# Kernel tuning notes

Measured on AMD Instinct MI355X. Metric: run time of the kernel, lower is better.

Reference implementation:

```python
import jax, jax.numpy as jnp
import numpy as np

N, E, C, Z, NB, NG, NL = 4000, 48000, 64, 10, 8, 8, 2
R_MAX = 5.0
P = 5.0  # polynomial cutoff power
AVG_NEIGH = 12.0
# l-index of each of the 16 spherical-harmonic components (l = 0..3)
ELLS = np.concatenate([[0], [1] * 3, [2] * 5, [3] * 7])


def _sph(u):
    # component-normalized real spherical harmonics up to l=3, u: unit vectors [E,3]
    x, y, z = u[..., 0], u[..., 1], u[..., 2]
    s3 = np.sqrt(3.0); s5 = np.sqrt(5.0); s15 = np.sqrt(15.0)
    s7 = np.sqrt(7.0); s105 = np.sqrt(105.0)
    s35_8 = np.sqrt(35.0 / 8.0); s21_8 = np.sqrt(21.0 / 8.0)
    x2, y2, z2 = x * x, y * y, z * z
    return jnp.stack([
        jnp.ones_like(x),
        s3 * x, s3 * y, s3 * z,
        s15 * x * y, s15 * y * z, 0.5 * s5 * (3.0 * z2 - 1.0), s15 * x * z, 0.5 * s15 * (x2 - y2),
        s35_8 * y * (3.0 * x2 - y2), s105 * x * y * z, s21_8 * y * (5.0 * z2 - 1.0),
        0.5 * s7 * z * (5.0 * z2 - 3.0), s21_8 * x * (5.0 * z2 - 1.0),
        0.5 * s105 * z * (x2 - y2), s35_8 * x * (x2 - 3.0 * y2),
    ], axis=-1)


def _radial(r):
    # Bessel radial basis * polynomial cutoff envelope; r: [E,1] -> [E,NB]
    n = jnp.arange(1, NB + 1, dtype=r.dtype)
    bess = np.sqrt(2.0 / R_MAX) * jnp.sin(n * jnp.pi * r / R_MAX) / r
    u = r / R_MAX
    env = 1.0 - 0.5 * (P + 1) * (P + 2) * u ** P + P * (P + 2) * u ** (P + 1) - 0.5 * P * (P + 1) * u ** (P + 2)
    env = jnp.where(u < 1.0, env, 0.0)
    return bess * env


def _per_l(f, W):
    # per-degree (l) channel mixing: f [N,C,16], W [4,C,C]
    return jnp.einsum('ncm,mcd->ndm', f, W[ELLS])


def _model(positions, x, shifts, W_embed, W_up, Wm1, Wm2, Wm3, W_out, W_sc, a_sc, w_poly, W_prod, w_r0, W_r1, w_r2, edge_index, batch):
    sender, receiver = edge_index[0], edge_index[1]
    vec = positions[receiver] - positions[sender] + shifts          # [E,3]
    length = jnp.sqrt(jnp.sum(vec * vec, axis=-1, keepdims=True))   # [E,1]
    edge_attrs = _sph(vec / length)                                 # [E,16]
    edge_feats = _radial(length)                                    # [E,NB]
    nf = jnp.zeros((N, C, 16), positions.dtype).at[:, :, 0].set(x @ W_embed)
    node_e = jnp.zeros((N,), positions.dtype)
    for i in range(NL):
        h = _per_l(nf, W_up[i])                                     # [N,C,16]
        w = jax.nn.silu(edge_feats @ Wm1[i])
        w = jax.nn.silu(w @ Wm2[i])
        w = (w @ Wm3[i]).reshape(E, C, 4)                           # per-(channel,l) radial weights
        h_s = h[:, :, 0][sender][:, :, None]                        # sender scalar feats [E,C,1]
        m = w[:, :, ELLS] * edge_attrs[:, None, :] * h_s            # messages [E,C,16]
        agg = jax.ops.segment_sum(m, receiver, num_segments=N) / AVG_NEIGH
        out = _per_l(agg, W_out[i])
        sc = _per_l(nf, W_sc[i]) * (x @ a_sc[i])[:, :, None]        # element-dependent skip
        s = out[:, :, 0]
        gate = w_poly[i, 0] + w_poly[i, 1] * s + w_poly[i, 2] * s * s  # correlation-3 scalar gate
        nf = _per_l(out * gate[:, :, None], W_prod[i]) + sc
        if i < NL - 1:
            node_e = node_e + nf[:, :, 0] @ w_r0
        else:
            node_e = node_e + jax.nn.silu(nf[:, :, 0] @ W_r1) @ w_r2
    snap = jax.ops.segment_sum(node_e, batch, num_segments=NG)
    return snap, node_e


def setup_inputs() -> dict:
    key = jax.random.key(0)
    ks = jax.random.split(key, 20)
    positions = jax.random.normal(ks[0], (N, 3), jnp.float32) * 3.0
    species = jax.random.randint(ks[1], (N,), 0, Z)
    x = jax.nn.one_hot(species, Z, dtype=jnp.float32)
    sender = jax.random.randint(ks[2], (E,), 0, N)
    offset = jax.random.randint(ks[3], (E,), 1, N)
    receiver = (sender + offset) % N  # no self loops -> length > 0
    edge_index = jnp.stack([sender, receiver]).astype(jnp.int32)
    shifts = jnp.zeros((E, 3), jnp.float32)
    batch = jnp.sort(jax.random.randint(ks[4], (N,), 0, NG)).astype(jnp.int32)
    g = lambda k, shp, scale: jax.random.normal(k, shp, jnp.float32) * scale
    inv = 1.0 / np.sqrt(C)
    return {
        'positions': positions, 'x': x, 'shifts': shifts,
        'W_embed': g(ks[5], (Z, C), 1.0 / np.sqrt(Z)),
        'W_up': g(ks[6], (NL, 4, C, C), inv),
        'Wm1': g(ks[7], (NL, NB, 64), 1.0 / np.sqrt(NB)),
        'Wm2': g(ks[8], (NL, 64, 64), 0.125),
        'Wm3': g(ks[9], (NL, 64, 4 * C), 0.125),
        'W_out': g(ks[10], (NL, 4, C, C), inv),
        'W_sc': g(ks[11], (NL, 4, C, C), inv),
        'a_sc': g(ks[12], (NL, Z, C), 1.0),
        'w_poly': g(ks[13], (NL, 3, C), 0.5),
        'W_prod': g(ks[14], (NL, 4, C, C), inv),
        'w_r0': g(ks[15], (C,), inv),
        'W_r1': g(ks[16], (C, 16), inv),
        'w_r2': g(ks[17], (16,), 0.25),
        'edge_index': edge_index, 'batch': batch,
    }


def reference(positions, x, shifts, W_embed, W_up, Wm1, Wm2, Wm3, W_out, W_sc, a_sc, w_poly, W_prod, w_r0, W_r1, w_r2, edge_index, batch):
    def efn(pos):
        snap, node_e = _model(pos, x, shifts, W_embed, W_up, Wm1, Wm2, Wm3, W_out, W_sc, a_sc, w_poly, W_prod, w_r0, W_r1, w_r2, edge_index, batch)
        return jnp.sum(snap), (snap, node_e)
    (_, (snap, node_e)), g = jax.value_and_grad(efn, has_aux=True)(positions)
    forces = -g
    return snap, node_e, forces
```

## Files before the change

### kernel.cpp

```cpp
#include <hip/hip_runtime.h>
#include <math.h>

constexpr int NN = 4000;
constexpr int EE = 48000;
constexpr int ZZ = 10;
constexpr float RMAX = 5.0f;
constexpr float INV_AVG = 1.0f / 12.0f;

constexpr int GB_EDGE = 188;
constexpr int GB_SPEC = GB_EDGE + 16;
constexpr int GB_W3Z  = GB_SPEC + 32;
constexpr int GB_T0   = GB_W3Z + 3;
constexpr int GB_ZERO = GB_T0 + 64;
constexpr int ZWS_F4  = 3*NN*64/4;
constexpr int ZOUT_F4 = 3*NN/4;

__device__ __forceinline__ float rl(float v, int lane){
    return __uint_as_float(__builtin_amdgcn_readlane(__float_as_uint(v), lane));
}
__device__ __forceinline__ float sigf(float x){ return 1.0f/(1.0f+__expf(-x)); }
__device__ __forceinline__ float siluf(float x){ return x*sigf(x); }
__device__ __forceinline__ float dsiluf(float x){ float s=sigf(x); return s*(1.0f+x*(1.0f-s)); }

__device__ __forceinline__ void pin64(float (&W)[64]){
#pragma unroll
    for (int i=0;i<64;i++) asm volatile("" : "+v"(W[i]));
}
__device__ __forceinline__ void pin8(float (&W)[8]){
#pragma unroll
    for (int i=0;i<8;i++) asm volatile("" : "+v"(W[i]));
}

__device__ __forceinline__ float bmv_s(const float* act, const float (&W)[64]){
    float a0=0.f,a1=0.f,a2=0.f,a3=0.f;
#pragma unroll
    for (int k=0;k<64;k+=4){
        a0 += act[k+0]*W[k+0];
        a1 += act[k+1]*W[k+1];
        a2 += act[k+2]*W[k+2];
        a3 += act[k+3]*W[k+3];
    }
    return (a0+a1)+(a2+a3);
}
__device__ __forceinline__ float bmv_lds(float v, const float (&W)[64], float* slice, int lane){
    slice[lane] = v;
    float a0=0.f,a1=0.f,a2=0.f,a3=0.f;
#pragma unroll
    for (int k=0;k<64;k+=4){
        float4 a = *reinterpret_cast<const float4*>(slice + k);
        a0 += a.x*W[k+0];
        a1 += a.y*W[k+1];
        a2 += a.z*W[k+2];
        a3 += a.w*W[k+3];
    }
    return (a0+a1)+(a2+a3);
}
__device__ __forceinline__ void load_row64(const float* __restrict__ p, float (&W)[64]){
#pragma unroll
    for (int i=0;i<16;i++){
        float4 v = reinterpret_cast<const float4*>(p)[i];
        W[4*i]=v.x; W[4*i+1]=v.y; W[4*i+2]=v.z; W[4*i+3]=v.w;
    }
}
__device__ __forceinline__ void load_col64(const float* __restrict__ p, int lane, float (&W)[64]){
#pragma unroll
    for (int k=0;k<64;k++) W[k] = p[k*64+lane];
}

__global__ void k_zero(int* __restrict__ ecount, float* __restrict__ out)
{
    int t = threadIdx.x;
    if (t < 8) out[t] = 0.0f;
    if (t == 8) *ecount = 0;
}

__global__ void k_geom(const float* __restrict__ pos, const float* __restrict__ shifts,
                       const int* __restrict__ ei, const float* __restrict__ x,
                       const float* __restrict__ WE, const float* __restrict__ W_up,
                       const float* __restrict__ W_sc, const float* __restrict__ a_sc,
                       const float* __restrict__ Wm3,
                       int* __restrict__ spec,
                       float* __restrict__ u3c, float* __restrict__ frc, float* __restrict__ dfrc,
                       int* __restrict__ esrc, int* __restrict__ edst, int* __restrict__ ecount,
                       float* __restrict__ T0, float* __restrict__ SC0, float* __restrict__ W3z,
                       float4* __restrict__ zws, float* __restrict__ out)
{
    int b = blockIdx.x;
    if (b >= GB_ZERO) return;
    if (b >= GB_T0){
        float4 z4 = make_float4(0.f,0.f,0.f,0.f);
        float4* zout = (float4*)(out + 8 + NN);
        for (int i=(b-GB_T0)*256 + threadIdx.x; i < ZWS_F4 + ZOUT_F4; i += 64*256){
            if (i < ZWS_F4) zws[i] = z4;
            else zout[i-ZWS_F4] = z4;
        }
        return;
    }
    if (b >= GB_W3Z){
        int wv = (b-GB_W3Z)*4 + (threadIdx.x>>6);
        int lane = threadIdx.x & 63;
        if (wv < ZZ){
            float wev = WE[wv*64 + lane];
            float t=0.f, sc=0.f;
#pragma unroll
            for (int c=0;c<64;c++){
                float w = rl(wev,c);
                t  += w*W_up[c*64+lane];
                sc += w*W_sc[c*64+lane];
            }
            T0[wv*64+lane]  = t;
            SC0[wv*64+lane] = sc * a_sc[wv*64+lane];
        }
        return;
    }
    if (b >= GB_SPEC){
        int idx = (b-GB_SPEC)*256 + threadIdx.x;
        int l = idx >> 12;
        int kc = idx & 4095;
        int k = kc >> 6, c = kc & 63;
        W3z[idx] = Wm3[l*64*256 + k*256 + 4*c];
        return;
    }
    if (b >= GB_EDGE){
        int n = (b-GB_EDGE)*256 + threadIdx.x;
        if (n < NN){
            int sp = 0;
#pragma unroll
            for (int j=0;j<ZZ;j++) if (x[n*ZZ+j] > 0.5f) sp = j;
            spec[n] = sp;
        }
        return;
    }
    int e = b*256 + threadIdx.x;
    if (e >= EE) return;
    int s = ei[e], r = ei[EE+e];
    float vx = pos[r*3+0]-pos[s*3+0]+shifts[e*3+0];
    float vy = pos[r*3+1]-pos[s*3+1]+shifts[e*3+1];
    float vz = pos[r*3+2]-pos[s*3+2]+shifts[e*3+2];
    float rr = sqrtf(vx*vx+vy*vy+vz*vz);
    float u = rr*(1.0f/RMAX);
    if (u >= 1.0f) return;
    int slot = atomicAdd(ecount, 1);
    esrc[slot]=s; edst[slot]=r;
    float inv = 1.0f/rr;
    u3c[slot*3+0]=vx*inv; u3c[slot*3+1]=vy*inv; u3c[slot*3+2]=vz*inv;
    float u2=u*u, u4=u2*u2, u5=u4*u;
    float env  = 1.0f - 21.0f*u5 + 35.0f*u5*u - 15.0f*u5*u2;
    float om   = 1.0f-u;
    float denv = -21.0f*u4*om*om;
    const float A = 0.6324555320336759f;
    const float K1 = 3.14159265358979f/RMAX;
    float a  = K1*rr;
    float s1 = __sinf(a), c1 = __cosf(a);
    float sp = 0.0f, cp = 1.0f, sn = s1, cn = c1;
#pragma unroll
    for (int n=1;n<=8;n++){
        float k = (float)n*K1;
        float bess  = A*sn*inv;
        float dbess = A*(k*cn - sn*inv)*inv;
        frc [slot*8+n-1] = bess*env;
        dfrc[slot*8+n-1] = dbess*env + bess*denv;
        float s2 = 2.0f*c1*sn - sp; sp=sn; sn=s2;
        float c2 = 2.0f*c1*cn - cp; cp=cn; cn=c2;
    }
}

template<int L>
__global__ __launch_bounds__(256,2)
void k_edge_fwd(const float* __restrict__ frc, const int* __restrict__ esrc,
                const int* __restrict__ edst, const int* __restrict__ ecount,
                const int* __restrict__ spec, const float* __restrict__ T0,
                const float* __restrict__ h1,
                const float* __restrict__ W1, const float* __restrict__ W2,
                const float* __restrict__ W3z,
                float* __restrict__ agg, float* __restrict__ t2b,
                float* __restrict__ w0b)
{
    __shared__ float sact[4][64];
    int lane = threadIdx.x & 63;
    float* slice = sact[threadIdx.x>>6];
    int wid  = (blockIdx.x*256 + threadIdx.x) >> 6;
    int nw   = gridDim.x*4;
    int cnt  = ecount[0];
    float W1c[8], W2c[64], W3c[64];
#pragma unroll
    for (int j=0;j<8;j++) W1c[j] = W1[j*64+lane];
    load_col64(W2,  lane, W2c);
    load_col64(W3z, lane, W3c);
    pin8(W1c); pin64(W2c); pin64(W3c);
    for (int slot=wid; slot<cnt; slot+=nw){
        int us = __builtin_amdgcn_readfirstlane(slot);
        int s = esrc[us], r = edst[us];
        const float* fn = frc + us*8;
        float t1=0.f;
#pragma unroll
        for (int j=0;j<8;j++) t1 += fn[j]*W1c[j];
        float t2 = bmv_lds(siluf(t1), W2c, slice, lane);
        t2b[(size_t)us*64+lane] = t2;
        float w0 = bmv_lds(siluf(t2), W3c, slice, lane);
        if (L==1) w0b[(size_t)us*64+lane] = w0;
        float h = (L==0) ? T0[spec[s]*64+lane] : h1[s*64+lane];
        atomicAdd(&agg[r*64+lane], w0*h*INV_AVG);
    }
}

__global__ __launch_bounds__(256,2)
void k_node_fwd0(const float* __restrict__ agg, const float* __restrict__ SC0,
                 const int* __restrict__ spec, const int* __restrict__ batch,
                 const float* __restrict__ Wout, const float* __restrict__ Wprod,
                 const float* __restrict__ Wup1, const float* __restrict__ poly,
                 const float* __restrict__ wr0,
                 float* __restrict__ s0, float* __restrict__ nf1,
                 float* __restrict__ h1, float* __restrict__ out)
{
    __shared__ float part[8];
    __shared__ float sact[4][64];
    if (threadIdx.x < 8) part[threadIdx.x] = 0.f;
    __syncthreads();
    int lane = threadIdx.x & 63;
    float* slice = sact[threadIdx.x>>6];
    int wid = (blockIdx.x*256 + threadIdx.x) >> 6;
    int nw  = gridDim.x*4;
    float WA[64], WB[64], WC[64];
    load_col64(Wout, lane, WA);
    load_col64(Wprod,lane, WB);
    load_col64(Wup1, lane, WC);
    pin64(WA); pin64(WB); pin64(WC);
    float p0=poly[lane], p1=poly[64+lane], p2=poly[128+lane];
    float w0r = wr0[lane];
    for (int nn=wid; nn<NN; nn+=nw){
        int n = __builtin_amdgcn_readfirstlane(nn);
        const float* an = agg + n*64;
        float s  = bmv_s(an, WA);
        float gate = p0 + p1*s + p2*s*s;
        float nf = bmv_lds(s*gate, WB, slice, lane) + SC0[spec[n]*64+lane];
        s0 [n*64+lane] = s;
        nf1[n*64+lane] = nf;
        h1 [n*64+lane] = bmv_lds(nf, WC, slice, lane);
        float ne = nf*w0r;
#pragma unroll
        for (int off=32;off;off>>=1) ne += __shfl_xor(ne,off);
        if (lane==0){ out[8+n] = ne; atomicAdd(&part[batch[n]], ne); }
    }
    __syncthreads();
    if (threadIdx.x < 8) atomicAdd(&out[threadIdx.x], part[threadIdx.x]);
}

__global__ __launch_bounds__(256,2)
void k_node_fwd1(const float* __restrict__ agg, const float* __restrict__ nf1,
                 const int* __restrict__ spec, const float* __restrict__ Wout,
                 const float* __restrict__ Wprod, const float* __restrict__ Wsc,
                 const float* __restrict__ asc, const float* __restrict__ poly,
                 float* __restrict__ s1, float* __restrict__ nf2)
{
    __shared__ float sact[4][64];
    int lane = threadIdx.x & 63;
    float* slice = sact[threadIdx.x>>6];
    int wid = (blockIdx.x*256 + threadIdx.x) >> 6;
    int nw  = gridDim.x*4;
    float Oc[64], Pc[64], Sc[64];
    load_col64(Wout, lane, Oc);
    load_col64(Wprod,lane, Pc);
    load_col64(Wsc,  lane, Sc);
    pin64(Oc); pin64(Pc); pin64(Sc);
    float p0=poly[lane], p1=poly[64+lane], p2=poly[128+lane];
    for (int nn=wid; nn<NN; nn+=nw){
        int n = __builtin_amdgcn_readfirstlane(nn);
        const float* an  = agg + n*64;
        const float* nfn = nf1 + n*64;
        float s   = bmv_s(an, Oc);
        float scp = bmv_s(nfn, Sc);
        float gate = p0 + p1*s + p2*s*s;
        float nf  = bmv_lds(s*gate, Pc, slice, lane) + scp*asc[spec[n]*64+lane];
        s1 [n*64+lane] = s;
        nf2[n*64+lane] = nf;
    }
}

__global__ __launch_bounds__(256,2)
void k_read1(const float* __restrict__ nf2, const int* __restrict__ batch,
             const float* __restrict__ Wr1, const float* __restrict__ wr2,
             float* __restrict__ out, float* __restrict__ gnf2)
{
    __shared__ float part[8];
    __shared__ float sact[4][64];
    if (threadIdx.x < 8) part[threadIdx.x] = 0.f;
    __syncthreads();
    int lane = threadIdx.x & 63;
    float* slice = sact[threadIdx.x>>6];
    int wid = (blockIdx.x*256 + threadIdx.x) >> 6;
    int nw  = gridDim.x*4;
    int j = lane & 15;
    float Wcol[64];
#pragma unroll
    for (int c=0;c<64;c++) Wcol[c] = Wr1[c*16 + j];
    pin64(Wcol);
    float Wrow[16];
#pragma unroll
    for (int i=0;i<4;i++){
        float4 v = reinterpret_cast<const float4*>(Wr1 + lane*16)[i];
        Wrow[4*i]=v.x; Wrow[4*i+1]=v.y; Wrow[4*i+2]=v.z; Wrow[4*i+3]=v.w;
    }
    float w2 = wr2[j];
    for (int nn=wid; nn<NN; nn+=nw){
        int n = __builtin_amdgcn_readfirstlane(nn);
        const float* nfn = nf2 + n*64;
        float z  = bmv_s(nfn, Wcol);
        float ne = siluf(z)*w2;
#pragma unroll
        for (int off=32;off;off>>=1) ne += __shfl_xor(ne,off);
        ne *= 0.25f;
        float gz = w2*dsiluf(z);
        slice[lane] = gz;
        float g = 0.f;
#pragma unroll
        for (int jj=0;jj<16;jj+=4){
            float4 a = *reinterpret_cast<const float4*>(slice + jj);
            g += a.x*Wrow[jj] + a.y*Wrow[jj+1] + a.z*Wrow[jj+2] + a.w*Wrow[jj+3];
        }
        gnf2[n*64+lane] = g;
        if (lane==0){ out[8+n] += ne; atomicAdd(&part[batch[n]], ne); }
    }
    __syncthreads();
    if (threadIdx.x < 8) atomicAdd(&out[threadIdx.x], part[threadIdx.x]);
}

__global__ __launch_bounds__(256,2)
void k_bnode1(const float* __restrict__ gin, const float* __restrict__ sbuf,
              const float* __restrict__ Wout, const float* __restrict__ Wprod,
              const float* __restrict__ Wsc, const float* __restrict__ asc,
              const int* __restrict__ spec, const float* __restrict__ poly,
              float* __restrict__ gagg, float* __restrict__ gsc)
{
    __shared__ float sact[4][64];
    int lane = threadIdx.x & 63;
    float* slice = sact[threadIdx.x>>6];
    int wid = (blockIdx.x*256 + threadIdx.x) >> 6;
    int nw  = gridDim.x*4;
    float Pr[64], Or[64], Sr[64];
    load_row64(Wprod + lane*64, Pr);
    load_row64(Wout  + lane*64, Or);
    load_row64(Wsc   + lane*64, Sr);
    pin64(Pr); pin64(Or); pin64(Sr);
    float p0=poly[lane], p1=poly[64+lane], p2=poly[128+lane];
    for (int nn=wid; nn<NN; nn+=nw){
        int n = __builtin_amdgcn_readfirstlane(nn);
        const float* gn = gin + n*64;
        float gv = bmv_s(gn, Pr);
        float s  = sbuf[n*64+lane];
        float gate = p0 + p1*s + p2*s*s;
        float gs = gv*(gate + s*(p1 + 2.0f*p2*s));
        gagg[n*64+lane] = bmv_lds(gs, Or, slice, lane);
        const float* ascn = asc + spec[n]*64;
        float a0=0.f,a1=0.f,a2=0.f,a3=0.f;
#pragma unroll
        for (int k=0;k<64;k+=4){
            a0 += (gn[k+0]*ascn[k+0])*Sr[k+0];
            a1 += (gn[k+1]*ascn[k+1])*Sr[k+1];
            a2 += (gn[k+2]*ascn[k+2])*Sr[k+2];
            a3 += (gn[k+3]*ascn[k+3])*Sr[k+3];
        }
        gsc[n*64+lane] = (a0+a1)+(a2+a3);
    }
}

__global__ __launch_bounds__(256,2)
void k_bnode0(const float* __restrict__ ghb, const float* __restrict__ gacc,
              const float* __restrict__ Wup1, const float* __restrict__ wr0,
              const float* __restrict__ sbuf, const float* __restrict__ Wout,
              const float* __restrict__ Wprod, const float* __restrict__ poly,
              float* __restrict__ gagg)
{
    __shared__ float sact[4][64];
    int lane = threadIdx.x & 63;
    float* slice = sact[threadIdx.x>>6];
    int wid = (blockIdx.x*256 + threadIdx.x) >> 6;
    int nw  = gridDim.x*4;
    float Ur[64], Pr[64], Or[64];
    load_row64(Wup1 + lane*64, Ur);
    load_row64(Wprod+ lane*64, Pr);
    load_row64(Wout + lane*64, Or);
    pin64(Ur); pin64(Pr); pin64(Or);
    float p0=poly[lane], p1=poly[64+lane], p2=poly[128+lane];
    float w0r = wr0[lane];
    for (int nn=wid; nn<NN; nn+=nw){
        int n = __builtin_amdgcn_readfirstlane(nn);
        const float* ghn = ghb + n*64;
        float g  = bmv_s(ghn, Ur) + gacc[n*64+lane] + w0r;
        float gv = bmv_lds(g, Pr, slice, lane);
        float s  = sbuf[n*64+lane];
        float gate = p0 + p1*s + p2*s*s;
        float gs = gv*(gate + s*(p1 + 2.0f*p2*s));
        gagg[n*64+lane] = bmv_lds(gs, Or, slice, lane);
    }
}

template<int L>
__global__ __launch_bounds__(256,2)
void k_edge_bwd(const float* __restrict__ frc, const float* __restrict__ dfrc,
                const float* __restrict__ u3c, const int* __restrict__ esrc,
                const int* __restrict__ edst, const int* __restrict__ ecount,
                const int* __restrict__ spec, const float* __restrict__ T0,
                const float* __restrict__ h1, const float* __restrict__ gagg,
                const float* __restrict__ t2b, const float* __restrict__ w0b,
                const float* __restrict__ W1, const float* __restrict__ W2,
                const float* __restrict__ W3z,
                float* __restrict__ ghb, float* __restrict__ out)
{
    __shared__ float sact[4][64];
    int lane = threadIdx.x & 63;
    float* slice = sact[threadIdx.x>>6];
    int wid  = (blockIdx.x*256 + threadIdx.x) >> 6;
    int nw   = gridDim.x*4;
    int cnt  = ecount[0];
    float* outf = out + 8 + NN;
    float W3r[64], W2r[64], W1c[8];
    load_row64(W3z + lane*64, W3r);
    load_row64(W2  + lane*64, W2r);
#pragma unroll
    for (int j=0;j<8;j++) W1c[j] = W1[j*64+lane];
    pin64(W3r); pin64(W2r); pin8(W1c);
    for (int slot=wid; slot<cnt; slot+=nw){
        int us = __builtin_amdgcn_readfirstlane(slot);
        int s = esrc[us], r = edst[us];
        float gm = gagg[r*64+lane]*INV_AVG;
        float h  = (L==0) ? T0[spec[s]*64+lane] : h1[s*64+lane];
        if (L==1) atomicAdd(&ghb[s*64+lane], gm*w0b[(size_t)us*64+lane]);
        float ga2 = bmv_lds(gm*h, W3r, slice, lane);
        float gt2 = ga2*dsiluf(t2b[(size_t)us*64+lane]);
        float ga1 = bmv_lds(gt2, W2r, slice, lane);
        const float* fn  = frc  + us*8;
        const float* dfn = dfrc + us*8;
        float t1=0.f, wd=0.f;
#pragma unroll
        for (int j=0;j<8;j++){ t1 += fn[j]*W1c[j]; wd += dfn[j]*W1c[j]; }
        float p = ga1*dsiluf(t1)*wd;
#pragma unroll
        for (int off=32;off;off>>=1) p += __shfl_xor(p,off);
        if (lane<3) atomicAdd(&outf[r*3+lane], -u3c[us*3+lane]*p);
        else if (lane>=32 && lane<35){ int d=lane-32; atomicAdd(&outf[s*3+d], u3c[us*3+d]*p); }
    }
}

extern "C" void kernel_launch(void* const* d_in, const int* in_sizes, int n_in,
                              void* d_out, int out_size, void* d_ws, size_t ws_size,
                              hipStream_t stream)
{
    (void)in_sizes; (void)n_in; (void)out_size; (void)ws_size;
    const float* pos    = (const float*)d_in[0];
    const float* x      = (const float*)d_in[1];
    const float* shifts = (const float*)d_in[2];
    const float* W_embed= (const float*)d_in[3];
    const float* W_up   = (const float*)d_in[4];
    const float* Wm1    = (const float*)d_in[5];
    const float* Wm2    = (const float*)d_in[6];
    const float* Wm3    = (const float*)d_in[7];
    const float* W_out  = (const float*)d_in[8];
    const float* W_sc   = (const float*)d_in[9];
    const float* a_sc   = (const float*)d_in[10];
    const float* w_poly = (const float*)d_in[11];
    const float* W_prod = (const float*)d_in[12];
    const float* w_r0   = (const float*)d_in[13];
    const float* W_r1   = (const float*)d_in[14];
    const float* w_r2   = (const float*)d_in[15];
    const int*   ei     = (const int*)d_in[16];
    const int*   batch  = (const int*)d_in[17];
    float* out = (float*)d_out;

    float* F = (float*)d_ws;
    float* agg0 = F; F += NN*64;
    float* agg1 = F; F += NN*64;
    float* ghb  = F; F += NN*64;
    int* ecount = (int*)F; F += 4;
    float* u3c  = F; F += 3*EE;
    float* frc  = F; F += 8*EE;
    float* dfrc = F; F += 8*EE;
    float* t2b0 = F; F += (size_t)EE*64;
    float* t2b1 = F; F += (size_t)EE*64;
    float* w0b1 = F; F += (size_t)EE*64;
    float* h1   = F; F += NN*64;
    float* nf1  = F; F += NN*64;
    float* nf2  = F; F += NN*64;
    float* s0   = F; F += NN*64;
    float* s1   = F; F += NN*64;
    float* gnf2 = F; F += NN*64;
    float* gagg1= F; F += NN*64;
    float* gagg0= F; F += NN*64;
    float* gacc = F; F += NN*64;
    float* T0   = F; F += ZZ*64;
    float* SC0  = F; F += ZZ*64;
    float* W3z  = F; F += 2*64*64;
    int* spec   = (int*)F; F += NN;
    int* esrc   = (int*)F; F += EE;
    int* edst   = (int*)F; F += EE;

    const float* U0 = W_up;           const float* U1 = W_up   + 4*64*64;
    const float* O0 = W_out;          const float* O1 = W_out  + 4*64*64;
    const float* S0w= W_sc;           const float* S1w= W_sc   + 4*64*64;
    const float* P0 = W_prod;         const float* P1 = W_prod + 4*64*64;
    const float* M1_0=Wm1,  *M1_1=Wm1+8*64;
    const float* M2_0=Wm2,  *M2_1=Wm2+64*64;
    const float* asc1=a_sc+ZZ*64;
    const float* pl0=w_poly, *pl1=w_poly+3*64;
    float* W3z0 = W3z; float* W3z1 = W3z + 64*64;

    k_zero<<<1, 256, 0, stream>>>(ecount, out);
    k_geom<<<GB_ZERO, 256, 0, stream>>>(pos, shifts, ei, x, W_embed, U0, S0w, a_sc, Wm3,
                                        spec, u3c, frc, dfrc, esrc, edst, ecount,
                                        T0, SC0, W3z, (float4*)d_ws, out);

    k_edge_fwd<0><<<512,256,0,stream>>>(frc, esrc, edst, ecount, spec, T0, nullptr,
                                        M1_0, M2_0, W3z0, agg0, t2b0, nullptr);
    k_node_fwd0<<<500,256,0,stream>>>(agg0, SC0, spec, batch, O0, P0, U1, pl0, w_r0,
                                      s0, nf1, h1, out);
    k_edge_fwd<1><<<512,256,0,stream>>>(frc, esrc, edst, ecount, spec, nullptr, h1,
                                        M1_1, M2_1, W3z1, agg1, t2b1, w0b1);
    k_node_fwd1<<<500,256,0,stream>>>(agg1, nf1, spec, O1, P1, S1w, asc1, pl1, s1, nf2);
    k_read1<<<500,256,0,stream>>>(nf2, batch, W_r1, w_r2, out, gnf2);

    k_bnode1<<<500,256,0,stream>>>(gnf2, s1, O1, P1, S1w, asc1, spec, pl1, gagg1, gacc);
    k_edge_bwd<1><<<512,256,0,stream>>>(frc, dfrc, u3c, esrc, edst, ecount, spec, nullptr, h1,
                                        gagg1, t2b1, w0b1, M1_1, M2_1, W3z1, ghb, out);
    k_bnode0<<<500,256,0,stream>>>(ghb, gacc, U1, w_r0, s0, O0, P0, pl0, gagg0);
    k_edge_bwd<0><<<512,256,0,stream>>>(frc, dfrc, u3c, esrc, edst, ecount, spec, T0, nullptr,
                                        gagg0, t2b0, nullptr, M1_0, M2_0, W3z0, nullptr, out);
}
```

Measured before the change: 156.0 us.

## Fuse layer-1 node forward, readout and backward into one kernel; pair edges per wave

Merges k_node_fwd1, k_read1 and k_bnode1 into a single k_node1 kernel in which each wave handles two fixed nodes (wid and wid+2000), keeping intermediates in registers instead of writing s1, nf2 and gnf2 to global memory. This drops two launches and the associated round trips. The edge forward and backward kernels now process two edges per wave iteration and use readlane-based matvecs instead of LDS staging, to expose ILP and remove LDS traffic. The node kernel relies on the exact grid (500 blocks × 4 waves = 2000) matching NN/2, and register pressure rises from holding two edges' state at once.

New measurement: 171.8 us. 1.1x slower.

```diff
diff --git a/kernel.cpp b/kernel.cpp
--- a/kernel.cpp
+++ b/kernel.cpp
@@ -31,6 +31,17 @@
     for (int i=0;i<8;i++) asm volatile("" : "+v"(W[i]));
 }
 
+__device__ __forceinline__ float bmv64(float src, const float (&W)[64]){
+    float a0=0.f,a1=0.f,a2=0.f,a3=0.f;
+#pragma unroll
+    for (int k=0;k<64;k+=4){
+        a0 += rl(src,k+0)*W[k+0];
+        a1 += rl(src,k+1)*W[k+1];
+        a2 += rl(src,k+2)*W[k+2];
+        a3 += rl(src,k+3)*W[k+3];
+    }
+    return (a0+a1)+(a2+a3);
+}
 __device__ __forceinline__ float bmv_s(const float* act, const float (&W)[64]){
     float a0=0.f,a1=0.f,a2=0.f,a3=0.f;
 #pragma unroll
@@ -176,9 +187,7 @@
                 float* __restrict__ agg, float* __restrict__ t2b,
                 float* __restrict__ w0b)
 {
-    __shared__ float sact[4][64];
     int lane = threadIdx.x & 63;
-    float* slice = sact[threadIdx.x>>6];
     int wid  = (blockIdx.x*256 + threadIdx.x) >> 6;
     int nw   = gridDim.x*4;
     int cnt  = ecount[0];
@@ -188,19 +197,34 @@
     load_col64(W2,  lane, W2c);
     load_col64(W3z, lane, W3c);
     pin8(W1c); pin64(W2c); pin64(W3c);
-    for (int slot=wid; slot<cnt; slot+=nw){
-        int us = __builtin_amdgcn_readfirstlane(slot);
-        int s = esrc[us], r = edst[us];
-        const float* fn = frc + us*8;
-        float t1=0.f;
-#pragma unroll
-        for (int j=0;j<8;j++) t1 += fn[j]*W1c[j];
-        float t2 = bmv_lds(siluf(t1), W2c, slice, lane);
-        t2b[(size_t)us*64+lane] = t2;
-        float w0 = bmv_lds(siluf(t2), W3c, slice, lane);
-        if (L==1) w0b[(size_t)us*64+lane] = w0;
-        float h = (L==0) ? T0[spec[s]*64+lane] : h1[s*64+lane];
-        atomicAdd(&agg[r*64+lane], w0*h*INV_AVG);
+    for (int slot=wid; slot<cnt; slot+=2*nw){
+        int usA = __builtin_amdgcn_readfirstlane(slot);
+        int slotB = slot + nw;
+        bool vB = slotB < cnt;
+        int usB = __builtin_amdgcn_readfirstlane(vB ? slotB : slot);
+        int sA = esrc[usA], rA = edst[usA];
+        int sB = esrc[usB], rB = edst[usB];
+        const float* fA = frc + usA*8;
+        const float* fB = frc + usB*8;
+        float t1A=0.f, t1B=0.f;
+#pragma unroll
+        for (int j=0;j<8;j++){ t1A += fA[j]*W1c[j]; t1B += fB[j]*W1c[j]; }
+        float a1A = siluf(t1A), a1B = siluf(t1B);
+        float t2A = bmv64(a1A, W2c);
+        float t2B = bmv64(a1B, W2c);
+        t2b[(size_t)usA*64+lane] = t2A;
+        if (vB) t2b[(size_t)usB*64+lane] = t2B;
+        float a2A = siluf(t2A), a2B = siluf(t2B);
+        float w0A = bmv64(a2A, W3c);
+        float w0B = bmv64(a2B, W3c);
+        if (L==1){
+            w0b[(size_t)usA*64+lane] = w0A;
+            if (vB) w0b[(size_t)usB*64+lane] = w0B;
+        }
+        float hA = (L==0) ? T0[spec[sA]*64+lane] : h1[sA*64+lane];
+        float hB = (L==0) ? T0[spec[sB]*64+lane] : h1[sB*64+lane];
+        atomicAdd(&agg[rA*64+lane], w0A*hA*INV_AVG);
+        if (vB) atomicAdd(&agg[rB*64+lane], w0B*hB*INV_AVG);
     }
 }
 
@@ -247,40 +271,13 @@
 }
 
 __global__ __launch_bounds__(256,2)
-void k_node_fwd1(const float* __restrict__ agg, const float* __restrict__ nf1,
-                 const int* __restrict__ spec, const float* __restrict__ Wout,
-                 const float* __restrict__ Wprod, const float* __restrict__ Wsc,
-                 const float* __restrict__ asc, const float* __restrict__ poly,
-                 float* __restrict__ s1, float* __restrict__ nf2)
-{
-    __shared__ float sact[4][64];
-    int lane = threadIdx.x & 63;
-    float* slice = sact[threadIdx.x>>6];
-    int wid = (blockIdx.x*256 + threadIdx.x) >> 6;
-    int nw  = gridDim.x*4;
-    float Oc[64], Pc[64], Sc[64];
-    load_col64(Wout, lane, Oc);
-    load_col64(Wprod,lane, Pc);
-    load_col64(Wsc,  lane, Sc);
-    pin64(Oc); pin64(Pc); pin64(Sc);
-    float p0=poly[lane], p1=poly[64+lane], p2=poly[128+lane];
-    for (int nn=wid; nn<NN; nn+=nw){
-        int n = __builtin_amdgcn_readfirstlane(nn);
-        const float* an  = agg + n*64;
-        const float* nfn = nf1 + n*64;
-        float s   = bmv_s(an, Oc);
-        float scp = bmv_s(nfn, Sc);
-        float gate = p0 + p1*s + p2*s*s;
-        float nf  = bmv_lds(s*gate, Pc, slice, lane) + scp*asc[spec[n]*64+lane];
-        s1 [n*64+lane] = s;
-        nf2[n*64+lane] = nf;
-    }
-}
-
-__global__ __launch_bounds__(256,2)
-void k_read1(const float* __restrict__ nf2, const int* __restrict__ batch,
-             const float* __restrict__ Wr1, const float* __restrict__ wr2,
-             float* __restrict__ out, float* __restrict__ gnf2)
+void k_node1(const float* __restrict__ agg, const float* __restrict__ nf1,
+             const int* __restrict__ spec, const int* __restrict__ batch,
+             const float* __restrict__ Wout, const float* __restrict__ Wprod,
+             const float* __restrict__ Wsc, const float* __restrict__ asc,
+             const float* __restrict__ poly, const float* __restrict__ Wr1,
+             const float* __restrict__ wr2,
+             float* __restrict__ out, float* __restrict__ gagg, float* __restrict__ gacc)
 {
     __shared__ float part[8];
     __shared__ float sact[4][64];
@@ -289,23 +286,37 @@
     int lane = threadIdx.x & 63;
     float* slice = sact[threadIdx.x>>6];
     int wid = (blockIdx.x*256 + threadIdx.x) >> 6;
-    int nw  = gridDim.x*4;
+    int na = __builtin_amdgcn_readfirstlane(wid);
+    int nb = na + 2000;
+    int spA = spec[na], spB = spec[nb];
+    float p0=poly[lane], p1=poly[64+lane], p2=poly[128+lane];
+    float WA[64], WB[64], WC[64];
+    load_col64(Wout, lane, WA);
+    load_col64(Wprod,lane, WB);
+    load_col64(Wsc,  lane, WC);
+    pin64(WA); pin64(WB); pin64(WC);
+    float sA = bmv_s(agg + na*64, WA);
+    float sB = bmv_s(agg + nb*64, WA);
+    float scpA = bmv_s(nf1 + na*64, WC);
+    float scpB = bmv_s(nf1 + nb*64, WC);
+    float gateA = p0 + p1*sA + p2*sA*sA;
+    float gateB = p0 + p1*sB + p2*sB*sB;
+    float nfA = bmv_lds(sA*gateA, WB, slice, lane) + scpA*asc[spA*64+lane];
+    float nfB = bmv_lds(sB*gateB, WB, slice, lane) + scpB*asc[spB*64+lane];
     int j = lane & 15;
-    float Wcol[64];
-#pragma unroll
-    for (int c=0;c<64;c++) Wcol[c] = Wr1[c*16 + j];
-    pin64(Wcol);
+    float w2 = wr2[j];
+#pragma unroll
+    for (int c=0;c<64;c++) WA[c] = Wr1[c*16 + j];
+    pin64(WA);
     float Wrow[16];
 #pragma unroll
-    for (int i=0;i<4;i++){
-        float4 v = reinterpret_cast<const float4*>(Wr1 + lane*16)[i];
-        Wrow[4*i]=v.x; Wrow[4*i+1]=v.y; Wrow[4*i+2]=v.z; Wrow[4*i+3]=v.w;
-    }
-    float w2 = wr2[j];
-    for (int nn=wid; nn<NN; nn+=nw){
-        int n = __builtin_amdgcn_readfirstlane(nn);
-        const float* nfn = nf2 + n*64;
-        float z  = bmv_s(nfn, Wcol);
+    for (int i2=0;i2<4;i2++){
+        float4 v = reinterpret_cast<const float4*>(Wr1 + lane*16)[i2];
+        Wrow[4*i2]=v.x; Wrow[4*i2+1]=v.y; Wrow[4*i2+2]=v.z; Wrow[4*i2+3]=v.w;
+    }
+    float gA, gB;
+    {
+        float z  = bmv_lds(nfA, WA, slice, lane);
         float ne = siluf(z)*w2;
 #pragma unroll
         for (int off=32;off;off>>=1) ne += __shfl_xor(ne,off);
@@ -318,50 +329,44 @@
             float4 a = *reinterpret_cast<const float4*>(slice + jj);
             g += a.x*Wrow[jj] + a.y*Wrow[jj+1] + a.z*Wrow[jj+2] + a.w*Wrow[jj+3];
         }
-        gnf2[n*64+lane] = g;
-        if (lane==0){ out[8+n] += ne; atomicAdd(&part[batch[n]], ne); }
+        gA = g;
+        if (lane==0){ out[8+na] += ne; atomicAdd(&part[batch[na]], ne); }
+    }
+    {
+        float z  = bmv_lds(nfB, WA, slice, lane);
+        float ne = siluf(z)*w2;
+#pragma unroll
+        for (int off=32;off;off>>=1) ne += __shfl_xor(ne,off);
+        ne *= 0.25f;
+        float gz = w2*dsiluf(z);
+        slice[lane] = gz;
+        float g = 0.f;
+#pragma unroll
+        for (int jj=0;jj<16;jj+=4){
+            float4 a = *reinterpret_cast<const float4*>(slice + jj);
+            g += a.x*Wrow[jj] + a.y*Wrow[jj+1] + a.z*Wrow[jj+2] + a.w*Wrow[jj+3];
+        }
+        gB = g;
+        if (lane==0){ out[8+nb] += ne; atomicAdd(&part[batch[nb]], ne); }
+    }
+    load_row64(Wprod + lane*64, WA);
+    load_row64(Wout  + lane*64, WB);
+    load_row64(Wsc   + lane*64, WC);
+    pin64(WA); pin64(WB); pin64(WC);
+    {
+        float gv = bmv_lds(gA, WA, slice, lane);
+        float gs = gv*(gateA + sA*(p1 + 2.0f*p2*sA));
+        gagg[na*64+lane] = bmv_lds(gs, WB, slice, lane);
+        gacc[na*64+lane] = bmv_lds(gA*asc[spA*64+lane], WC, slice, lane);
+    }
+    {
+        float gv = bmv_lds(gB, WA, slice, lane);
+        float gs = gv*(gateB + sB*(p1 + 2.0f*p2*sB));
+        gagg[nb*64+lane] = bmv_lds(gs, WB, slice, lane);
+        gacc[nb*64+lane] = bmv_lds(gB*asc[spB*64+lane], WC, slice, lane);
     }
     __syncthreads();
     if (threadIdx.x < 8) atomicAdd(&out[threadIdx.x], part[threadIdx.x]);
-}
-
-__global__ __launch_bounds__(256,2)
-void k_bnode1(const float* __restrict__ gin, const float* __restrict__ sbuf,
-              const float* __restrict__ Wout, const float* __restrict__ Wprod,
-              const float* __restrict__ Wsc, const float* __restrict__ asc,
-              const int* __restrict__ spec, const float* __restrict__ poly,
-              float* __restrict__ gagg, float* __restrict__ gsc)
-{
-    __shared__ float sact[4][64];
-    int lane = threadIdx.x & 63;
-    float* slice = sact[threadIdx.x>>6];
-    int wid = (blockIdx.x*256 + threadIdx.x) >> 6;
-    int nw  = gridDim.x*4;
-    float Pr[64], Or[64], Sr[64];
-    load_row64(Wprod + lane*64, Pr);
-    load_row64(Wout  + lane*64, Or);
-    load_row64(Wsc   + lane*64, Sr);
-    pin64(Pr); pin64(Or); pin64(Sr);
-    float p0=poly[lane], p1=poly[64+lane], p2=poly[128+lane];
-    for (int nn=wid; nn<NN; nn+=nw){
-        int n = __builtin_amdgcn_readfirstlane(nn);
-        const float* gn = gin + n*64;
-        float gv = bmv_s(gn, Pr);
-        float s  = sbuf[n*64+lane];
-        float gate = p0 + p1*s + p2*s*s;
-        float gs = gv*(gate + s*(p1 + 2.0f*p2*s));
-        gagg[n*64+lane] = bmv_lds(gs, Or, slice, lane);
-        const float* ascn = asc + spec[n]*64;
-        float a0=0.f,a1=0.f,a2=0.f,a3=0.f;
-#pragma unroll
-        for (int k=0;k<64;k+=4){
-            a0 += (gn[k+0]*ascn[k+0])*Sr[k+0];
-            a1 += (gn[k+1]*ascn[k+1])*Sr[k+1];
-            a2 += (gn[k+2]*ascn[k+2])*Sr[k+2];
-            a3 += (gn[k+3]*ascn[k+3])*Sr[k+3];
-        }
-        gsc[n*64+lane] = (a0+a1)+(a2+a3);
-    }
 }
 
 __global__ __launch_bounds__(256,2)
@@ -407,9 +412,7 @@
                 const float* __restrict__ W3z,
                 float* __restrict__ ghb, float* __restrict__ out)
 {
-    __shared__ float sact[4][64];
     int lane = threadIdx.x & 63;
-    float* slice = sact[threadIdx.x>>6];
     int wid  = (blockIdx.x*256 + threadIdx.x) >> 6;
     int nw   = gridDim.x*4;
     int cnt  = ecount[0];
@@ -420,25 +423,47 @@
 #pragma unroll
     for (int j=0;j<8;j++) W1c[j] = W1[j*64+lane];
     pin64(W3r); pin64(W2r); pin8(W1c);
-    for (int slot=wid; slot<cnt; slot+=nw){
-        int us = __builtin_amdgcn_readfirstlane(slot);
-        int s = esrc[us], r = edst[us];
-        float gm = gagg[r*64+lane]*INV_AVG;
-        float h  = (L==0) ? T0[spec[s]*64+lane] : h1[s*64+lane];
-        if (L==1) atomicAdd(&ghb[s*64+lane], gm*w0b[(size_t)us*64+lane]);
-        float ga2 = bmv_lds(gm*h, W3r, slice, lane);
-        float gt2 = ga2*dsiluf(t2b[(size_t)us*64+lane]);
-        float ga1 = bmv_lds(gt2, W2r, slice, lane);
-        const float* fn  = frc  + us*8;
-        const float* dfn = dfrc + us*8;
-        float t1=0.f, wd=0.f;
-#pragma unroll
-        for (int j=0;j<8;j++){ t1 += fn[j]*W1c[j]; wd += dfn[j]*W1c[j]; }
-        float p = ga1*dsiluf(t1)*wd;
-#pragma unroll
-        for (int off=32;off;off>>=1) p += __shfl_xor(p,off);
-        if (lane<3) atomicAdd(&outf[r*3+lane], -u3c[us*3+lane]*p);
-        else if (lane>=32 && lane<35){ int d=lane-32; atomicAdd(&outf[s*3+d], u3c[us*3+d]*p); }
+    for (int slot=wid; slot<cnt; slot+=2*nw){
+        int usA = __builtin_amdgcn_readfirstlane(slot);
+        int slotB = slot + nw;
+        bool vB = slotB < cnt;
+        int usB = __builtin_amdgcn_readfirstlane(vB ? slotB : slot);
+        int sA = esrc[usA], rA = edst[usA];
+        int sB = esrc[usB], rB = edst[usB];
+        float gmA = gagg[rA*64+lane]*INV_AVG;
+        float gmB = gagg[rB*64+lane]*INV_AVG;
+        float hA  = (L==0) ? T0[spec[sA]*64+lane] : h1[sA*64+lane];
+        float hB  = (L==0) ? T0[spec[sB]*64+lane] : h1[sB*64+lane];
+        if (L==1){
+            atomicAdd(&ghb[sA*64+lane], gmA*w0b[(size_t)usA*64+lane]);
+            if (vB) atomicAdd(&ghb[sB*64+lane], gmB*w0b[(size_t)usB*64+lane]);
+        }
+        float ga2A = bmv64(gmA*hA, W3r);
+        float ga2B = bmv64(gmB*hB, W3r);
+        float gt2A = ga2A*dsiluf(t2b[(size_t)usA*64+lane]);
+        float gt2B = ga2B*dsiluf(t2b[(size_t)usB*64+lane]);
+        float ga1A = bmv64(gt2A, W2r);
+        float ga1B = bmv64(gt2B, W2r);
+        const float* fA  = frc  + usA*8;
+        const float* dfA = dfrc + usA*8;
+        const float* fB  = frc  + usB*8;
+        const float* dfB = dfrc + usB*8;
+        float t1A=0.f, wdA=0.f, t1B=0.f, wdB=0.f;
+#pragma unroll
+        for (int j=0;j<8;j++){
+            t1A += fA[j]*W1c[j]; wdA += dfA[j]*W1c[j];
+            t1B += fB[j]*W1c[j]; wdB += dfB[j]*W1c[j];
+        }
+        float pA = ga1A*dsiluf(t1A)*wdA;
+        float pB = ga1B*dsiluf(t1B)*wdB;
+#pragma unroll
+        for (int off=32;off;off>>=1){ pA += __shfl_xor(pA,off); pB += __shfl_xor(pB,off); }
+        if (lane<3) atomicAdd(&outf[rA*3+lane], -u3c[usA*3+lane]*pA);
+        else if (lane>=32 && lane<35){ int d=lane-32; atomicAdd(&outf[sA*3+d], u3c[usA*3+d]*pA); }
+        if (vB){
+            if (lane<3) atomicAdd(&outf[rB*3+lane], -u3c[usB*3+lane]*pB);
+            else if (lane>=32 && lane<35){ int d=lane-32; atomicAdd(&outf[sB*3+d], u3c[usB*3+d]*pB); }
+        }
     }
 }
 
@@ -480,10 +505,7 @@
     float* w0b1 = F; F += (size_t)EE*64;
     float* h1   = F; F += NN*64;
     float* nf1  = F; F += NN*64;
-    float* nf2  = F; F += NN*64;
     float* s0   = F; F += NN*64;
-    float* s1   = F; F += NN*64;
-    float* gnf2 = F; F += NN*64;
     float* gagg1= F; F += NN*64;
     float* gagg0= F; F += NN*64;
     float* gacc = F; F += NN*64;
@@ -515,10 +537,9 @@
                                       s0, nf1, h1, out);
     k_edge_fwd<1><<<512,256,0,stream>>>(frc, esrc, edst, ecount, spec, nullptr, h1,
                                         M1_1, M2_1, W3z1, agg1, t2b1, w0b1);
-    k_node_fwd1<<<500,256,0,stream>>>(agg1, nf1, spec, O1, P1, S1w, asc1, pl1, s1, nf2);
-    k_read1<<<500,256,0,stream>>>(nf2, batch, W_r1, w_r2, out, gnf2);
-
-    k_bnode1<<<500,256,0,stream>>>(gnf2, s1, O1, P1, S1w, asc1, spec, pl1, gagg1, gacc);
+    k_node1<<<500,256,0,stream>>>(agg1, nf1, spec, batch, O1, P1, S1w, asc1, pl1,
+                                  W_r1, w_r2, out, gagg1, gacc);
+
     k_edge_bwd<1><<<512,256,0,stream>>>(frc, dfrc, u3c, esrc, edst, ecount, spec, nullptr, h1,
                                         gagg1, t2b1, w0b1, M1_1, M2_1, W3z1, ghb, out);
     k_bnode0<<<500,256,0,stream>>>(ghb, gacc, U1, w_r0, s0, O0, P0, pl0, gagg0);
```
